# Performance work log

Hardware: AMD Instinct MI355X
Metric: run time of the kernel (lower is better)

## Reference

```python
import jax, jax.numpy as jnp
import numpy as np

HIDDEN = 2880
NUM_EXPERTS = 32
TOP_K = 4


def setup_inputs() -> dict:
    key = jax.random.key(0)
    k1, k2, k3 = jax.random.split(key, 3)
    hidden_states = jax.random.normal(k1, (4, 4096, HIDDEN), dtype=jnp.float32)
    weight = jax.random.normal(k2, (NUM_EXPERTS, HIDDEN), dtype=jnp.float32) * (1.0 / np.sqrt(HIDDEN))
    bias = jax.random.normal(k3, (NUM_EXPERTS,), dtype=jnp.float32) * 0.02
    return {"hidden_states": hidden_states, "weight": weight, "bias": bias}


def reference(hidden_states, weight, bias):
    # flatten tokens: [T, H]
    x = hidden_states.reshape(-1, HIDDEN)
    # router logits: [T, E]
    router_logits = jnp.einsum('th,eh->te', x, weight) + bias
    # top-k selection along experts
    top_vals, top_idx = jax.lax.top_k(router_logits, TOP_K)  # [T, K]
    top_vals = jax.nn.softmax(top_vals, axis=-1)
    # scatter normalized scores back into a zero [T, E] tensor
    T = router_logits.shape[0]
    rows = jnp.arange(T)[:, None]
    router_scores = jnp.zeros_like(router_logits).at[rows, top_idx].set(top_vals)
    return router_scores, top_idx
```

## Files before the change

kernel.cpp:

```cpp
#include <hip/hip_runtime.h>
#include <math.h>


#define HIDDEN 2880
#define NE 32
#define TOPK 4
#define TPB 32
#define KSLOTS 96
#define VS (KSLOTS * 2 * 512)

typedef __attribute__((ext_vector_type(8))) short bf16x8;
typedef __attribute__((ext_vector_type(4))) float f32x4;

#define MFMA(a, b, c) __builtin_amdgcn_mfma_f32_16x16x32_bf16((a), (b), (c), 0, 0, 0)

__global__ void wb_kernel(const float* __restrict__ w, unsigned short* __restrict__ wb) {
    int i = blockIdx.x * 256 + threadIdx.x;
    if (i >= 3 * VS) return;
    int j = i & 7;
    int t = i >> 3;
    int l = t & 63;  t >>= 6;
    int et = t & 1;  t >>= 1;
    int ks = t % KSLOTS;
    int ver = t / KSLOTS;
    unsigned short outv = 0;
    if (ks < 90) {
        int e = et * 16 + (l & 15);
        int k = ks * 32 + (l >> 4) * 8 + j;
        float v = w[e * HIDDEN + k];
        unsigned u = __float_as_uint(v);
        unsigned h = u >> 16;
        float r = v - __uint_as_float(u & 0xffff0000u);
        unsigned ur = __float_as_uint(r);
        unsigned m = ur >> 16;
        float r2 = r - __uint_as_float(ur & 0xffff0000u);
        unsigned lo = __float_as_uint(r2) >> 16;
        outv = (unsigned short)(ver == 0 ? h : (ver == 1 ? m : lo));
    }
    wb[i] = outv;
}

__device__ __forceinline__ void split24(float4 a, float4 b,
                                        bf16x8& H, bf16x8& M, bf16x8& L) {
    union { bf16x8 v; unsigned u[4]; } h, m, l;
    float f[8] = {a.x, a.y, a.z, a.w, b.x, b.y, b.z, b.w};
    unsigned hh[8], mm[8], ll[8];
#pragma unroll
    for (int i = 0; i < 8; ++i) {
        unsigned u = __float_as_uint(f[i]);
        hh[i] = u >> 16;
        float r = f[i] - __uint_as_float(u & 0xffff0000u);
        unsigned ur = __float_as_uint(r);
        mm[i] = ur >> 16;
        float r2 = r - __uint_as_float(ur & 0xffff0000u);
        ll[i] = __float_as_uint(r2) >> 16;
    }
#pragma unroll
    for (int i = 0; i < 4; ++i) {
        h.u[i] = hh[2 * i] | (hh[2 * i + 1] << 16);
        m.u[i] = mm[2 * i] | (mm[2 * i + 1] << 16);
        l.u[i] = ll[2 * i] | (ll[2 * i + 1] << 16);
    }
    H = h.v; M = m.v; L = l.v;
}

__global__ __launch_bounds__(512, 4)
void router_kernel(const float* __restrict__ x,
                   const unsigned short* __restrict__ wb,
                   const float* __restrict__ bias,
                   float* __restrict__ out_scores,
                   float* __restrict__ out_idx)
{
    __shared__ float part[4][TPB][36];
    __shared__ float score[TPB][33];

    const int tid  = threadIdx.x;
    const int lane = tid & 63;
    const int w    = tid >> 6;
    const int wm   = w & 1;
    const int kq   = w >> 1;
    const int tl   = lane & 15;
    const int kb   = lane >> 4;

    const float* xrow = x + (size_t)(blockIdx.x * TPB + wm * 16 + tl) * HIDDEN + kb * 8;
    const unsigned short* wk = wb + lane * 8;

    f32x4 acc0 = {0.f, 0.f, 0.f, 0.f};
    f32x4 acc1 = {0.f, 0.f, 0.f, 0.f};

#define LOADX(A0, A1, sg) do {                                                    \
    const int sx_ = min((sg), 89);                                                \
    A0 = *(const float4*)(xrow + (size_t)sx_ * 32);                               \
    A1 = *(const float4*)(xrow + (size_t)sx_ * 32 + 4);                           \
} while (0)

#define LOADW(W, sg) do {                                                         \
    const unsigned short* p_ = wk + (size_t)min((sg), 95) * 1024;                 \
    W[0] = *(const bf16x8*)(p_);                          \
    W[1] = *(const bf16x8*)(p_ + 512);                    \
    W[2] = *(const bf16x8*)(p_ + VS);                     \
    W[3] = *(const bf16x8*)(p_ + VS + 512);               \
    W[4] = *(const bf16x8*)(p_ + 2 * VS);                 \
    W[5] = *(const bf16x8*)(p_ + 2 * VS + 512);           \
} while (0)

#define MFMA12(W, XH, XM, XL) do {                                                \
    acc0 = MFMA(W[0], XH, acc0);                                                  \
    acc1 = MFMA(W[1], XH, acc1);                                                  \
    acc0 = MFMA(W[2], XH, acc0);                                                  \
    acc1 = MFMA(W[3], XH, acc1);                                                  \
    acc0 = MFMA(W[4], XH, acc0);                                                  \
    acc1 = MFMA(W[5], XH, acc1);                                                  \
    acc0 = MFMA(W[0], XM, acc0);                                                  \
    acc1 = MFMA(W[1], XM, acc1);                                                  \
    acc0 = MFMA(W[2], XM, acc0);                                                  \
    acc1 = MFMA(W[3], XM, acc1);                                                  \
    acc0 = MFMA(W[0], XL, acc0);                                                  \
    acc1 = MFMA(W[1], XL, acc1);                                                  \
} while (0)

    const int sg0 = kq * 24;
    float4 xa0, xa1, xb0, xb1;
    bf16x8 Wa[6], Wb[6];
    LOADX(xa0, xa1, sg0);     LOADW(Wa, sg0);
    LOADX(xb0, xb1, sg0 + 1); LOADW(Wb, sg0 + 1);

#pragma unroll 1
    for (int i = 0; i < 12; ++i) {
        const int s = sg0 + 2 * i;
        {
            bf16x8 xh, xm, xl;
            split24(xa0, xa1, xh, xm, xl);
            LOADX(xa0, xa1, s + 2);
            MFMA12(Wa, xh, xm, xl);
            LOADW(Wa, s + 2);
        }
        {
            bf16x8 xh, xm, xl;
            split24(xb0, xb1, xh, xm, xl);
            LOADX(xb0, xb1, s + 3);
            MFMA12(Wb, xh, xm, xl);
            LOADW(Wb, s + 3);
        }
    }

#undef LOADX
#undef LOADW
#undef MFMA12

    {
        const int eb = (lane >> 4) * 4;
        *(f32x4*)&part[kq][wm * 16 + tl][eb]      = acc0;
        *(f32x4*)&part[kq][wm * 16 + tl][16 + eb] = acc1;
    }
    __syncthreads();

    if (tid < TPB) {
        float lg[NE];
#pragma unroll
        for (int e = 0; e < NE; ++e)
            lg[e] = part[0][tid][e] + part[1][tid][e]
                  + part[2][tid][e] + part[3][tid][e] + bias[e];

        float vals[TOPK]; int idxs[TOPK]; unsigned chosen = 0u;
#pragma unroll
        for (int k = 0; k < TOPK; ++k) {
            float m = -INFINITY; int mi = 0;
#pragma unroll
            for (int e = 0; e < NE; ++e) {
                const bool take = (((chosen >> e) & 1u) == 0u) && (lg[e] > m);
                m  = take ? lg[e] : m;
                mi = take ? e : mi;
            }
            vals[k] = m; idxs[k] = mi; chosen |= (1u << (unsigned)mi);
        }
        const float mx = vals[0];
        float p[TOPK]; float sum = 0.f;
#pragma unroll
        for (int k = 0; k < TOPK; ++k) { p[k] = __expf(vals[k] - mx); sum += p[k]; }
        const float inv = 1.0f / sum;
#pragma unroll
        for (int e = 0; e < NE; ++e) {
            float v = 0.f;
#pragma unroll
            for (int k = 0; k < TOPK; ++k) v = (e == idxs[k]) ? p[k] * inv : v;
            score[tid][e] = v;
        }
        const int t = blockIdx.x * TPB + tid;
        float4 iv = make_float4((float)idxs[0], (float)idxs[1], (float)idxs[2], (float)idxs[3]);
        *reinterpret_cast<float4*>(out_idx + (size_t)t * TOPK) = iv;
    }
    __syncthreads();

    {
        const int f = tid * 2;
        const int t = f >> 5, e = f & 31;
        float2 v = make_float2(score[t][e], score[t][e + 1]);
        *reinterpret_cast<float2*>(out_scores + (size_t)blockIdx.x * TPB * NE + f) = v;
    }
}

extern "C" void kernel_launch(void* const* d_in, const int* in_sizes, int n_in,
                              void* d_out, int out_size, void* d_ws, size_t ws_size,
                              hipStream_t stream)
{
    const float* x = (const float*)d_in[0];
    const float* w = (const float*)d_in[1];
    const float* b = (const float*)d_in[2];
    const int T = in_sizes[0] / HIDDEN;

    unsigned short* wbuf = (unsigned short*)d_ws;
    float* out        = (float*)d_out;
    float* out_scores = out;
    float* out_idx    = out + (size_t)T * NE;

    wb_kernel<<<dim3((3 * VS + 255) / 256), dim3(256), 0, stream>>>(w, wbuf);
    router_kernel<<<dim3(T / TPB), dim3(512), 0, stream>>>(x, wbuf, b, out_scores, out_idx);
}
```

Baseline: 56.14 us.

## Switch router GEMM to 32x32x16 MFMA with full-K-split across eight waves

Replaces the pair of 16x16x32 bf16 MFMAs (two expert halves, two token halves per wave) with a single 32x32x16 MFMA covering all 32 tokens and 32 experts, so each wave now owns a distinct K range and the block splits K eight ways instead of four. The weight prepack layout changes to match, and per-step weight loads drop from six vectors to three. The final reduction sums eight partials in shared memory instead of four. Out-of-range prefetches on the last iteration are skipped. The larger MFMA shape has a different issue latency and register footprint, so throughput per wave may shift.

```diff
diff --git a/kernel.cpp b/kernel.cpp
--- a/kernel.cpp
+++ b/kernel.cpp
@@ -6,27 +6,27 @@
 #define NE 32
 #define TOPK 4
 #define TPB 32
-#define KSLOTS 96
-#define VS (KSLOTS * 2 * 512)
-
-typedef __attribute__((ext_vector_type(8))) short bf16x8;
-typedef __attribute__((ext_vector_type(4))) float f32x4;
-
-#define MFMA(a, b, c) __builtin_amdgcn_mfma_f32_16x16x32_bf16((a), (b), (c), 0, 0, 0)
+#define NK16 192
+#define RK16 180
+#define VS (NK16 * 512)
+
+typedef __attribute__((ext_vector_type(8)))  short bf16x8;
+typedef __attribute__((ext_vector_type(16))) float f32x16;
+
+#define MFMA32(a, b, c) __builtin_amdgcn_mfma_f32_32x32x16_bf16((a), (b), (c), 0, 0, 0)
 
 __global__ void wb_kernel(const float* __restrict__ w, unsigned short* __restrict__ wb) {
     int i = blockIdx.x * 256 + threadIdx.x;
     if (i >= 3 * VS) return;
     int j = i & 7;
-    int t = i >> 3;
-    int l = t & 63;  t >>= 6;
-    int et = t & 1;  t >>= 1;
-    int ks = t % KSLOTS;
-    int ver = t / KSLOTS;
+    int l = (i >> 3) & 63;
+    int rest = i >> 9;
+    int ks  = rest % NK16;
+    int ver = rest / NK16;
     unsigned short outv = 0;
-    if (ks < 90) {
-        int e = et * 16 + (l & 15);
-        int k = ks * 32 + (l >> 4) * 8 + j;
+    if (ks < RK16) {
+        int e = l & 31;
+        int k = ks * 16 + (l >> 5) * 8 + j;
         float v = w[e * HIDDEN + k];
         unsigned u = __float_as_uint(v);
         unsigned h = u >> 16;
@@ -71,57 +71,45 @@
                    float* __restrict__ out_scores,
                    float* __restrict__ out_idx)
 {
-    __shared__ float part[4][TPB][36];
+    __shared__ float part[8][TPB][36];
     __shared__ float score[TPB][33];
 
     const int tid  = threadIdx.x;
     const int lane = tid & 63;
     const int w    = tid >> 6;
-    const int wm   = w & 1;
-    const int kq   = w >> 1;
-    const int tl   = lane & 15;
-    const int kb   = lane >> 4;
-
-    const float* xrow = x + (size_t)(blockIdx.x * TPB + wm * 16 + tl) * HIDDEN + kb * 8;
+    const int col  = lane & 31;
+    const int kg   = lane >> 5;
+
+    const float* xrow = x + (size_t)(blockIdx.x * TPB + col) * HIDDEN + kg * 8;
     const unsigned short* wk = wb + lane * 8;
 
-    f32x4 acc0 = {0.f, 0.f, 0.f, 0.f};
-    f32x4 acc1 = {0.f, 0.f, 0.f, 0.f};
+    f32x16 acc = {0.f};
 
 #define LOADX(A0, A1, sg) do {                                                    \
-    const int sx_ = min((sg), 89);                                                \
-    A0 = *(const float4*)(xrow + (size_t)sx_ * 32);                               \
-    A1 = *(const float4*)(xrow + (size_t)sx_ * 32 + 4);                           \
+    const int sx_ = min((sg), RK16 - 1);                                          \
+    A0 = *(const float4*)(xrow + (size_t)sx_ * 16);                               \
+    A1 = *(const float4*)(xrow + (size_t)sx_ * 16 + 4);                           \
 } while (0)
 
-#define LOADW(W, sg) do {                                                         \
-    const unsigned short* p_ = wk + (size_t)min((sg), 95) * 1024;                 \
-    W[0] = *(const bf16x8*)(p_);                          \
-    W[1] = *(const bf16x8*)(p_ + 512);                    \
-    W[2] = *(const bf16x8*)(p_ + VS);                     \
-    W[3] = *(const bf16x8*)(p_ + VS + 512);               \
-    W[4] = *(const bf16x8*)(p_ + 2 * VS);                 \
-    W[5] = *(const bf16x8*)(p_ + 2 * VS + 512);           \
+#define LOADW(W3, sg) do {                                                        \
+    const unsigned short* p_ = wk + (size_t)(sg) * 512;                           \
+    W3[0] = *(const bf16x8*)(p_);                                        \
+    W3[1] = *(const bf16x8*)(p_ + VS);                                   \
+    W3[2] = *(const bf16x8*)(p_ + 2 * VS);                               \
 } while (0)
 
-#define MFMA12(W, XH, XM, XL) do {                                                \
-    acc0 = MFMA(W[0], XH, acc0);                                                  \
-    acc1 = MFMA(W[1], XH, acc1);                                                  \
-    acc0 = MFMA(W[2], XH, acc0);                                                  \
-    acc1 = MFMA(W[3], XH, acc1);                                                  \
-    acc0 = MFMA(W[4], XH, acc0);                                                  \
-    acc1 = MFMA(W[5], XH, acc1);                                                  \
-    acc0 = MFMA(W[0], XM, acc0);                                                  \
-    acc1 = MFMA(W[1], XM, acc1);                                                  \
-    acc0 = MFMA(W[2], XM, acc0);                                                  \
-    acc1 = MFMA(W[3], XM, acc1);                                                  \
-    acc0 = MFMA(W[0], XL, acc0);                                                  \
-    acc1 = MFMA(W[1], XL, acc1);                                                  \
+#define MFMA6(W3, XH, XM, XL) do {                                                \
+    acc = MFMA32(W3[0], XH, acc);                                                 \
+    acc = MFMA32(W3[1], XH, acc);                                                 \
+    acc = MFMA32(W3[2], XH, acc);                                                 \
+    acc = MFMA32(W3[0], XM, acc);                                                 \
+    acc = MFMA32(W3[1], XM, acc);                                                 \
+    acc = MFMA32(W3[0], XL, acc);                                                 \
 } while (0)
 
-    const int sg0 = kq * 24;
+    const int sg0 = w * 24;
     float4 xa0, xa1, xb0, xb1;
-    bf16x8 Wa[6], Wb[6];
+    bf16x8 Wa[3], Wb[3];
     LOADX(xa0, xa1, sg0);     LOADW(Wa, sg0);
     LOADX(xb0, xb1, sg0 + 1); LOADW(Wb, sg0 + 1);
 
@@ -131,36 +119,37 @@
         {
             bf16x8 xh, xm, xl;
             split24(xa0, xa1, xh, xm, xl);
-            LOADX(xa0, xa1, s + 2);
-            MFMA12(Wa, xh, xm, xl);
-            LOADW(Wa, s + 2);
+            if (i < 11) LOADX(xa0, xa1, s + 2);
+            MFMA6(Wa, xh, xm, xl);
+            if (i < 11) LOADW(Wa, s + 2);
         }
         {
             bf16x8 xh, xm, xl;
             split24(xb0, xb1, xh, xm, xl);
-            LOADX(xb0, xb1, s + 3);
-            MFMA12(Wb, xh, xm, xl);
-            LOADW(Wb, s + 3);
+            if (i < 11) LOADX(xb0, xb1, s + 3);
+            MFMA6(Wb, xh, xm, xl);
+            if (i < 11) LOADW(Wb, s + 3);
         }
     }
 
 #undef LOADX
 #undef LOADW
-#undef MFMA12
-
-    {
-        const int eb = (lane >> 4) * 4;
-        *(f32x4*)&part[kq][wm * 16 + tl][eb]      = acc0;
-        *(f32x4*)&part[kq][wm * 16 + tl][16 + eb] = acc1;
-    }
+#undef MFMA6
+
+#pragma unroll
+    for (int r = 0; r < 16; ++r)
+        part[w][col][(r & 3) + 8 * (r >> 2) + 4 * kg] = acc[r];
     __syncthreads();
 
     if (tid < TPB) {
         float lg[NE];
 #pragma unroll
-        for (int e = 0; e < NE; ++e)
-            lg[e] = part[0][tid][e] + part[1][tid][e]
-                  + part[2][tid][e] + part[3][tid][e] + bias[e];
+        for (int e = 0; e < NE; ++e) {
+            float s = bias[e];
+#pragma unroll
+            for (int p = 0; p < 8; ++p) s += part[p][tid][e];
+            lg[e] = s;
+        }
 
         float vals[TOPK]; int idxs[TOPK]; unsigned chosen = 0u;
 #pragma unroll
```

Measured after the change: 54.95 us. 2.1% less time.

## Stage x through per-wave LDS tiles with coalesced row loads

Applied to the files above, without the earlier changes.

Activation rows are no longer read straight from global memory in the MFMA fragment pattern, where each lane took 32 bytes from a different row. Each wave now loads 64-float chunks of its 16 rows with coalesced 8-lanes-per-row float4 loads and writes them to a padded per-wave LDS tile. It then reads the MFMA fragments back from LDS, with the next chunk's global loads in flight. Launch bounds occupancy drops from 4 to 2 blocks to give registers room, and the kernel now uses about 35 KB more LDS per block.

```diff
diff --git a/kernel.cpp b/kernel.cpp
--- a/kernel.cpp
+++ b/kernel.cpp
@@ -8,6 +8,7 @@
 #define TPB 32
 #define KSLOTS 96
 #define VS (KSLOTS * 2 * 512)
+#define ROWF 68
 
 typedef __attribute__((ext_vector_type(8))) short bf16x8;
 typedef __attribute__((ext_vector_type(4))) float f32x4;
@@ -64,13 +65,14 @@
     H = h.v; M = m.v; L = l.v;
 }
 
-__global__ __launch_bounds__(512, 4)
+__global__ __launch_bounds__(512, 2)
 void router_kernel(const float* __restrict__ x,
                    const unsigned short* __restrict__ wb,
                    const float* __restrict__ bias,
                    float* __restrict__ out_scores,
                    float* __restrict__ out_idx)
 {
+    __shared__ float xt[8 * 16 * ROWF];
     __shared__ float part[4][TPB][36];
     __shared__ float score[TPB][33];
 
@@ -80,73 +82,94 @@
     const int wm   = w & 1;
     const int kq   = w >> 1;
     const int tl   = lane & 15;
-    const int kb   = lane >> 4;
-
-    const float* xrow = x + (size_t)(blockIdx.x * TPB + wm * 16 + tl) * HIDDEN + kb * 8;
+
+    float* tile = xt + w * (16 * ROWF);
+
+    const int srow  = lane >> 3;
+    const int sslot = lane & 7;
+    const float* xs0 = x + (size_t)(blockIdx.x * TPB + wm * 16 + srow) * HIDDEN + sslot * 4;
+    const float* xs1 = xs0 + (size_t)8 * HIDDEN;
+    float* sd0 = tile + srow * ROWF + sslot * 4;
+    float* sd1 = tile + (8 + srow) * ROWF + sslot * 4;
+
     const unsigned short* wk = wb + lane * 8;
+    const int kbase = kq * 768;
+    const int ks0   = kq * 24;
+    const int rbase = tl * ROWF + (lane >> 4) * 8;
 
     f32x4 acc0 = {0.f, 0.f, 0.f, 0.f};
     f32x4 acc1 = {0.f, 0.f, 0.f, 0.f};
 
-#define LOADX(A0, A1, sg) do {                                                    \
-    const int sx_ = min((sg), 89);                                                \
-    A0 = *(const float4*)(xrow + (size_t)sx_ * 32);                               \
-    A1 = *(const float4*)(xrow + (size_t)sx_ * 32 + 4);                           \
-} while (0)
-
-#define LOADW(W, sg) do {                                                         \
-    const unsigned short* p_ = wk + (size_t)min((sg), 95) * 1024;                 \
-    W[0] = *(const bf16x8*)(p_);                          \
-    W[1] = *(const bf16x8*)(p_ + 512);                    \
-    W[2] = *(const bf16x8*)(p_ + VS);                     \
-    W[3] = *(const bf16x8*)(p_ + VS + 512);               \
-    W[4] = *(const bf16x8*)(p_ + 2 * VS);                 \
-    W[5] = *(const bf16x8*)(p_ + 2 * VS + 512);           \
-} while (0)
-
-#define MFMA12(W, XH, XM, XL) do {                                                \
-    acc0 = MFMA(W[0], XH, acc0);                                                  \
-    acc1 = MFMA(W[1], XH, acc1);                                                  \
-    acc0 = MFMA(W[2], XH, acc0);                                                  \
-    acc1 = MFMA(W[3], XH, acc1);                                                  \
-    acc0 = MFMA(W[4], XH, acc0);                                                  \
-    acc1 = MFMA(W[5], XH, acc1);                                                  \
-    acc0 = MFMA(W[0], XM, acc0);                                                  \
-    acc1 = MFMA(W[1], XM, acc1);                                                  \
-    acc0 = MFMA(W[2], XM, acc0);                                                  \
-    acc1 = MFMA(W[3], XM, acc1);                                                  \
-    acc0 = MFMA(W[0], XL, acc0);                                                  \
-    acc1 = MFMA(W[1], XL, acc1);                                                  \
-} while (0)
-
-    const int sg0 = kq * 24;
-    float4 xa0, xa1, xb0, xb1;
-    bf16x8 Wa[6], Wb[6];
-    LOADX(xa0, xa1, sg0);     LOADW(Wa, sg0);
-    LOADX(xb0, xb1, sg0 + 1); LOADW(Wb, sg0 + 1);
+    float4 g0, g1, g2, g3;
+    bf16x8 Wa0, Wa1, Wa2, Wa3, Wa4, Wa5;
+    bf16x8 Wb0, Wb1, Wb2, Wb3, Wb4, Wb5;
+
+#define GLOADC(c) do {                                                            \
+    const int ko_ = min(kbase + 64 * (c), HIDDEN - 64);                           \
+    g0 = *(const float4*)(xs0 + ko_);                                             \
+    g1 = *(const float4*)(xs1 + ko_);                                             \
+    g2 = *(const float4*)(xs0 + ko_ + 32);                                        \
+    g3 = *(const float4*)(xs1 + ko_ + 32);                                        \
+} while (0)
+
+#define SWRITE() do {                                                             \
+    *(float4*)(sd0)      = g0;                                                    \
+    *(float4*)(sd1)      = g1;                                                    \
+    *(float4*)(sd0 + 32) = g2;                                                    \
+    *(float4*)(sd1 + 32) = g3;                                                    \
+} while (0)
+
+#define LOADW(W0, W1, W2, W3, W4, W5, sg) do {                                    \
+    const unsigned short* p_ = wk + (size_t)min((sg), KSLOTS - 1) * 1024;         \
+    W0 = *(const bf16x8*)(p_);                                      \
+    W1 = *(const bf16x8*)(p_ + 512);                                \
+    W2 = *(const bf16x8*)(p_ + VS);                                 \
+    W3 = *(const bf16x8*)(p_ + VS + 512);                           \
+    W4 = *(const bf16x8*)(p_ + 2 * VS);                             \
+    W5 = *(const bf16x8*)(p_ + 2 * VS + 512);                       \
+} while (0)
+
+#define STEP(st, W0, W1, W2, W3, W4, W5) do {                                     \
+    float4 a0_ = *(const float4*)(tile + rbase + (st) * 32);                      \
+    float4 a1_ = *(const float4*)(tile + rbase + (st) * 32 + 4);                  \
+    bf16x8 xh_, xm_, xl_;                                                         \
+    split24(a0_, a1_, xh_, xm_, xl_);                                             \
+    acc0 = MFMA(W0, xh_, acc0);                                                   \
+    acc1 = MFMA(W1, xh_, acc1);                                                   \
+    acc0 = MFMA(W2, xh_, acc0);                                                   \
+    acc1 = MFMA(W3, xh_, acc1);                                                   \
+    acc0 = MFMA(W4, xh_, acc0);                                                   \
+    acc1 = MFMA(W5, xh_, acc1);                                                   \
+    acc0 = MFMA(W0, xm_, acc0);                                                   \
+    acc1 = MFMA(W1, xm_, acc1);                                                   \
+    acc0 = MFMA(W2, xm_, acc0);                                                   \
+    acc1 = MFMA(W3, xm_, acc1);                                                   \
+    acc0 = MFMA(W0, xl_, acc0);                                                   \
+    acc1 = MFMA(W1, xl_, acc1);                                                   \
+} while (0)
+
+    GLOADC(0);
+    SWRITE();
+    GLOADC(1);
+    LOADW(Wa0, Wa1, Wa2, Wa3, Wa4, Wa5, ks0);
+    LOADW(Wb0, Wb1, Wb2, Wb3, Wb4, Wb5, ks0 + 1);
 
 #pragma unroll 1
-    for (int i = 0; i < 12; ++i) {
-        const int s = sg0 + 2 * i;
-        {
-            bf16x8 xh, xm, xl;
-            split24(xa0, xa1, xh, xm, xl);
-            LOADX(xa0, xa1, s + 2);
-            MFMA12(Wa, xh, xm, xl);
-            LOADW(Wa, s + 2);
+    for (int c = 0; c < 12; ++c) {
+        STEP(0, Wa0, Wa1, Wa2, Wa3, Wa4, Wa5);
+        LOADW(Wa0, Wa1, Wa2, Wa3, Wa4, Wa5, ks0 + 2 * c + 2);
+        STEP(1, Wb0, Wb1, Wb2, Wb3, Wb4, Wb5);
+        LOADW(Wb0, Wb1, Wb2, Wb3, Wb4, Wb5, ks0 + 2 * c + 3);
+        if (c < 11) {
+            SWRITE();
+            GLOADC(c + 2);
         }
-        {
-            bf16x8 xh, xm, xl;
-            split24(xb0, xb1, xh, xm, xl);
-            LOADX(xb0, xb1, s + 3);
-            MFMA12(Wb, xh, xm, xl);
-            LOADW(Wb, s + 3);
-        }
-    }
-
-#undef LOADX
+    }
+
+#undef GLOADC
+#undef SWRITE
 #undef LOADW
-#undef MFMA12
+#undef STEP
 
     {
         const int eb = (lane >> 4) * 4;
```

Measured after the change: 52.21 us. 1.08x faster.
